# Performance work log

Measured on AMD Instinct MI355X. Metric: run time of the kernel, lower is better.

## Reference

```python
import jax, jax.numpy as jnp
import numpy as np

DIM = 64
DIM_BAK = 64
WIN = 8
HEADS = 4
HEAD_DIM = DIM // HEADS
SCALE = HEAD_DIM ** -0.5


def setup_inputs() -> dict:
    key = jax.random.key(0)
    ks = jax.random.split(key, 10)
    b, h, w = 8, 256, 256
    inp = {
        "query_feature": jax.random.normal(ks[0], (b, DIM, h, w), jnp.float32),
        "key_value_feature": jax.random.normal(ks[1], (b, DIM_BAK, h, w), jnp.float32),
        # Linear weights stored as (in, out); torch nn.Linear is y = x @ W.T + b
        "wq": jax.random.normal(ks[2], (DIM, DIM), jnp.float32) * 0.02,
        "bq": jnp.zeros((DIM,), jnp.float32),
        "wkv": jax.random.normal(ks[3], (DIM_BAK, 2 * DIM), jnp.float32) * 0.02,
        "bkv": jnp.zeros((2 * DIM,), jnp.float32),
        # depthwise 3x3 conv, groups=DIM_BAK, no bias; OIHW with I=1
        "w_dw": jax.random.normal(ks[4], (DIM_BAK, 1, 3, 3), jnp.float32) * 0.1,
        "w_out": jax.random.normal(ks[5], (DIM, DIM), jnp.float32) * 0.02,
        "b_out": jnp.zeros((DIM,), jnp.float32),
    }
    return inp


def _window_partition(x_nhwc, ws):
    # [B,H,W,C] -> [B*(H/ws)*(W/ws), ws*ws, C]
    B, H, W, C = x_nhwc.shape
    x = x_nhwc.reshape(B, H // ws, ws, W // ws, ws, C)
    x = x.transpose(0, 1, 3, 2, 4, 5)
    return x.reshape(-1, ws * ws, C)


def _window_reverse(win, ws, B, H, W):
    # [B*(H/ws)*(W/ws), ws, ws, C] -> [B,H,W,C]
    C = win.shape[-1]
    x = win.reshape(B, H // ws, W // ws, ws, ws, C)
    x = x.transpose(0, 1, 3, 2, 4, 5)
    return x.reshape(B, H, W, C)


def reference(query_feature, key_value_feature, wq, bq, wkv, bkv, w_dw, w_out, b_out):
    b, c, h, w = query_feature.shape
    c2 = key_value_feature.shape[1]

    # depthwise 3x3 conv on kv feature (NCHW)
    kv_feat = jax.lax.conv_general_dilated(
        key_value_feature, w_dw, window_strides=(1, 1), padding="SAME",
        dimension_numbers=("NCHW", "OIHW", "NCHW"), feature_group_count=c2)

    q_win = _window_partition(query_feature.transpose(0, 2, 3, 1), WIN)   # [B_, N, c]
    kv_win = _window_partition(kv_feat.transpose(0, 2, 3, 1), WIN)        # [B_, N, c2]
    B_, N, _ = q_win.shape

    q = (q_win @ wq + bq).reshape(B_, N, HEADS, HEAD_DIM).transpose(0, 2, 1, 3) * SCALE
    kv = (kv_win @ wkv + bkv).reshape(B_, N, 2, HEADS, HEAD_DIM).transpose(2, 0, 3, 1, 4)
    k, v = kv[0], kv[1]                                                   # [B_, H, N, hd]

    attn = jax.nn.softmax(jnp.einsum("bhnd,bhmd->bhnm", q, k), axis=-1)
    out = jnp.einsum("bhnm,bhmd->bhnd", attn, v)
    out = out.transpose(0, 2, 1, 3).reshape(B_, N, HEADS * HEAD_DIM)
    out = out @ w_out + b_out

    out = _window_reverse(out.reshape(-1, WIN, WIN, c), WIN, b, h, w)
    return out.transpose(0, 3, 1, 2)  # NCHW
```

## Files before the change

### kernel.cpp

```cpp
#include <hip/hip_runtime.h>
#include <hip/hip_bf16.h>

typedef __bf16 bf16x8 __attribute__((ext_vector_type(8)));
typedef float  f32x4  __attribute__((ext_vector_type(4)));
typedef short  s16x4  __attribute__((ext_vector_type(4)));

#define QSCALE 0.25f
#define LOG2E  1.4426950408889634f

static __device__ __forceinline__ unsigned short f2bf(float x) {
  union { __bf16 h; unsigned short u; } c;
  c.h = (__bf16)x;
  return c.u;
}
static __device__ __forceinline__ unsigned pk2(float a, float b) {
  union { __bf16 h[2]; unsigned u; } c;
  c.h[0] = (__bf16)a; c.h[1] = (__bf16)b;
  return c.u;
}
static __device__ __forceinline__ s16x4 mk4(unsigned w0, unsigned w1) {
  union { unsigned u[2]; s16x4 v; } c; c.u[0] = w0; c.u[1] = w1; return c.v;
}

#define SWZ(tk, ch2b) ((unsigned)((tk) * 128 + ((ch2b) ^ (((tk) & 7) << 4))))
#define OFFQ 15360u
#define OFFC 23552u

__global__ void prep_weights(const float* __restrict__ wq, const float* __restrict__ wkv,
                             const float* __restrict__ wout, const float* __restrict__ bq,
                             const float* __restrict__ bkv, const float* __restrict__ bout,
                             const float* __restrict__ wdw, unsigned* __restrict__ ws32) {
  const unsigned t = threadIdx.x;
  for (unsigned e = t; e < 2048; e += 256) {
    const unsigned fid = e >> 6, lane = e & 63;
    const unsigned l15 = lane & 15, g = lane >> 4;
    float v[8];
    if (fid < 8) {
      const unsigned nt = fid >> 1, kt = fid & 1, n = nt * 16 + l15;
#pragma unroll
      for (int i = 0; i < 8; ++i) v[i] = wq[(kt * 32 + g * 8 + i) * 64 + n] * (QSCALE * LOG2E);
    } else if (fid < 24) {
      const unsigned f = fid - 8, nt = f >> 1, kt = f & 1, n = nt * 16 + l15;
#pragma unroll
      for (int i = 0; i < 8; ++i) v[i] = wkv[(kt * 32 + g * 8 + i) * 128 + n];
    } else {
      const unsigned f = fid - 24, mt = f >> 1, kt = f & 1, m = mt * 16 + l15;
#pragma unroll
      for (int i = 0; i < 8; ++i) v[i] = wout[(kt * 32 + g * 8 + i) * 64 + m];
    }
#pragma unroll
    for (int w = 0; w < 4; ++w) ws32[e * 4 + w] = pk2(v[2 * w], v[2 * w + 1]);
  }
  float* bws = (float*)(ws32 + 8192);
  if (t < 64)       bws[t] = bq[t] * (QSCALE * LOG2E);
  else if (t < 192) bws[t] = bkv[t - 64];
  else if (t < 256) bws[t] = bout[t - 192];
  float* wT = (float*)(ws32 + 8448);
  for (unsigned e = t; e < 576; e += 256) {
    const unsigned k = e >> 6, ch = e & 63;
    wT[k * 64 + ch] = wdw[ch * 9 + k];
  }
}

__launch_bounds__(256, 5)
__global__ void fused_win_attn(const float* __restrict__ qf, const float* __restrict__ kvf,
                               const unsigned* __restrict__ ws32, float* __restrict__ out) {
  __shared__ __align__(16) char lds[31744];
  unsigned short* lds16 = (unsigned short*)lds;
  unsigned* lds32p = (unsigned*)lds;

  const unsigned bid = blockIdx.x;
  const unsigned wid = (bid & 7) * 1024 + (bid >> 3);
  const unsigned b = wid >> 10, rem = wid & 1023;
  const unsigned y0 = (rem >> 5) * 8, x0 = (rem & 31) * 8;

  const unsigned t = threadIdx.x;
  const unsigned lane = t & 63;
  const unsigned wv = t >> 6;
  const unsigned l15 = lane & 15, g = lane >> 4;
  const f32x4 zero4 = (f32x4){0.f, 0.f, 0.f, 0.f};

#pragma unroll
  for (int k = 0; k < 4; ++k) {
    const unsigned slot = (unsigned)k * 256 + t, seg = slot >> 1, part = slot & 1;
    const unsigned ch = seg >> 3, row = seg & 7;
    const f32x4 v = *(const f32x4*)(qf + ((size_t)b * 64 + ch) * 65536
                                    + (size_t)(y0 + row) * 256 + x0 + part * 4);
#pragma unroll
    for (int i = 0; i < 4; ++i)
      lds16[(OFFQ + SWZ(row * 8 + part * 4 + (unsigned)i, ch * 2)) >> 1] = f2bf(v[i]);
  }

#pragma unroll
  for (int k = 0; k < 10; ++k) {
    const unsigned slot = (unsigned)k * 256 + t, seg = slot >> 2, p4 = slot & 3;
    const unsigned irow = seg >> 6, ch = seg & 63;
    const int yy = (int)(y0 + irow) - 1;
    const int xs = (int)x0 - 4 + (int)p4 * 4;
    f32x4 v = zero4;
    if (yy >= 0 && yy < 256 && xs >= 0 && xs + 3 < 256)
      v = *(const f32x4*)(kvf + ((size_t)b * 64 + ch) * 65536 + (size_t)yy * 256 + xs);
    const unsigned base = irow * 384;
    if (p4 == 0) {
      lds32p[base + 0 * 64 + (ch & 63)]        = pk2(v[2], v[3]);
    } else if (p4 == 1) {
      lds32p[base + 1 * 64 + ((ch + 4) & 63)]  = pk2(v[0], v[1]);
      lds32p[base + 2 * 64 + ((ch + 8) & 63)]  = pk2(v[2], v[3]);
    } else if (p4 == 2) {
      lds32p[base + 3 * 64 + ((ch + 12) & 63)] = pk2(v[0], v[1]);
      lds32p[base + 4 * 64 + ((ch + 16) & 63)] = pk2(v[2], v[3]);
    } else {
      lds32p[base + 5 * 64 + ((ch + 20) & 63)] = pk2(v[0], v[1]);
    }
  }
  __syncthreads();

  {
    const unsigned ch = lane;
    const float* wT = (const float*)(ws32 + 8448);
    float wgt[9];
#pragma unroll
    for (int k2 = 0; k2 < 9; ++k2) wgt[k2] = wT[k2 * 64 + ch];
    float acc[2][8];
#pragma unroll
    for (int o = 0; o < 2; ++o)
#pragma unroll
      for (int c = 0; c < 8; ++c) acc[o][c] = 0.f;
#pragma unroll
    for (int il = 0; il < 4; ++il) {
      const unsigned irow = 2 * wv + (unsigned)il;
      float x[12];
#pragma unroll
      for (int j = 0; j < 6; ++j) {
        const unsigned u = lds32p[irow * 384 + (unsigned)j * 64 + ((ch + 4 * (unsigned)j) & 63)];
        x[2 * j]     = __uint_as_float(u << 16);
        x[2 * j + 1] = __uint_as_float(u & 0xffff0000u);
      }
#pragma unroll
      for (int o = 0; o < 2; ++o) {
        const int dr = il - o;
        if (dr >= 0 && dr <= 2) {
#pragma unroll
          for (int c = 0; c < 8; ++c)
            acc[o][c] = fmaf(x[c + 1], wgt[dr * 3],
                        fmaf(x[c + 2], wgt[dr * 3 + 1],
                        fmaf(x[c + 3], wgt[dr * 3 + 2], acc[o][c])));
        }
      }
    }
#pragma unroll
    for (int o = 0; o < 2; ++o)
#pragma unroll
      for (int c = 0; c < 8; ++c)
        lds16[(OFFC + SWZ((2 * wv + (unsigned)o) * 8 + (unsigned)c, ch * 2)) >> 1] =
            f2bf(acc[o][c]);
  }
  __syncthreads();

  const bf16x8* wsf = (const bf16x8*)ws32;
  const float* bws = (const float*)(ws32 + 8192);

  f32x4 qT[4], kT[4], vN[4];
  {
    const f32x4 bq4 = (f32x4){bws[wv * 16 + g * 4 + 0], bws[wv * 16 + g * 4 + 1],
                              bws[wv * 16 + g * 4 + 2], bws[wv * 16 + g * 4 + 3]};
    const f32x4 bk4 = (f32x4){bws[64 + wv * 16 + g * 4 + 0], bws[64 + wv * 16 + g * 4 + 1],
                              bws[64 + wv * 16 + g * 4 + 2], bws[64 + wv * 16 + g * 4 + 3]};
    const float bvv = bws[128 + wv * 16 + l15];
#pragma unroll
    for (int nt = 0; nt < 4; ++nt) {
      qT[nt] = bq4; kT[nt] = bk4;
      vN[nt] = (f32x4){bvv, bvv, bvv, bvv};
    }
#pragma unroll
    for (int kt = 0; kt < 2; ++kt) {
      const bf16x8 wqA = wsf[(wv * 2 + kt) * 64 + lane];
      const bf16x8 wkA = wsf[512 + (wv * 2 + kt) * 64 + lane];
      const bf16x8 wvB = wsf[512 + ((4 + wv) * 2 + kt) * 64 + lane];
#pragma unroll
      for (int nt = 0; nt < 4; ++nt) {
        const unsigned byo = SWZ(nt * 16 + l15, (kt * 32 + g * 8) * 2);
        const bf16x8 qF  = *(const bf16x8*)(lds + OFFQ + byo);
        const bf16x8 kvF = *(const bf16x8*)(lds + OFFC + byo);
        qT[nt] = __builtin_amdgcn_mfma_f32_16x16x32_bf16(wqA, qF,  qT[nt], 0, 0, 0);
        kT[nt] = __builtin_amdgcn_mfma_f32_16x16x32_bf16(wkA, kvF, kT[nt], 0, 0, 0);
        vN[nt] = __builtin_amdgcn_mfma_f32_16x16x32_bf16(kvF, wvB, vN[nt], 0, 0, 0);
      }
    }
  }

  unsigned ka[4][2], qa[4][2], va[4][2];
#pragma unroll
  for (int t4 = 0; t4 < 4; ++t4) {
    ka[t4][0] = pk2(kT[t4][0], kT[t4][1]); ka[t4][1] = pk2(kT[t4][2], kT[t4][3]);
    qa[t4][0] = pk2(qT[t4][0], qT[t4][1]); qa[t4][1] = pk2(qT[t4][2], qT[t4][3]);
    va[t4][0] = pk2(vN[t4][0], vN[t4][1]); va[t4][1] = pk2(vN[t4][2], vN[t4][3]);
  }

#pragma unroll
  for (int nt = 0; nt < 4; ++nt) {
    f32x4 s[4];
#pragma unroll
    for (int mt = 0; mt < 4; ++mt)
      s[mt] = __builtin_amdgcn_mfma_f32_16x16x16bf16_1k(
          mk4(ka[mt][0], ka[mt][1]), mk4(qa[nt][0], qa[nt][1]), zero4, 0, 0, 0);
    float m = s[0][0];
#pragma unroll
    for (int mt = 0; mt < 4; ++mt)
#pragma unroll
      for (int r = 0; r < 4; ++r) m = fmaxf(m, s[mt][r]);
    m = fmaxf(m, __shfl_xor(m, 16));
    m = fmaxf(m, __shfl_xor(m, 32));
    float sum = 0.f;
#pragma unroll
    for (int mt = 0; mt < 4; ++mt)
#pragma unroll
      for (int r = 0; r < 4; ++r) {
        const float e = exp2f(s[mt][r] - m);
        s[mt][r] = e;
        sum += e;
      }
    sum += __shfl_xor(sum, 16);
    sum += __shfl_xor(sum, 32);
    const float sinv = 1.0f / sum;
    f32x4 o = zero4;
#pragma unroll
    for (int k2 = 0; k2 < 4; ++k2)
      o = __builtin_amdgcn_mfma_f32_16x16x16bf16_1k(
          mk4(va[k2][0], va[k2][1]),
          mk4(pk2(s[k2][0], s[k2][1]), pk2(s[k2][2], s[k2][3])), o, 0, 0, 0);
#pragma unroll
    for (int r = 0; r < 4; ++r)
      lds16[SWZ(nt * 16 + l15, (wv * 16 + g * 4 + r) * 2) >> 1] = f2bf(o[r] * sinv);
  }
  __syncthreads();

  float bo[4];
#pragma unroll
  for (int r = 0; r < 4; ++r) bo[r] = bws[192 + wv * 16 + g * 4 + r];
  f32x4 facc[4];
#pragma unroll
  for (int nt = 0; nt < 4; ++nt) facc[nt] = (f32x4){bo[0], bo[1], bo[2], bo[3]};
#pragma unroll
  for (int kt = 0; kt < 2; ++kt) {
    const bf16x8 woA = wsf[1536 + (wv * 2 + kt) * 64 + lane];
#pragma unroll
    for (int nt = 0; nt < 4; ++nt) {
      const bf16x8 aB = *(const bf16x8*)(lds + SWZ(nt * 16 + l15, (kt * 32 + g * 8) * 2));
      facc[nt] = __builtin_amdgcn_mfma_f32_16x16x32_bf16(woA, aB, facc[nt], 0, 0, 0);
    }
  }
  float* ob = out + (size_t)b * 4194304 + (size_t)(wv * 16) * 65536 + (size_t)y0 * 256 + x0;
#pragma unroll
  for (int nt = 0; nt < 4; ++nt)
#pragma unroll
    for (int r = 0; r < 4; ++r) {
      const unsigned tk = nt * 16 + l15;
      ob[(size_t)(g * 4 + r) * 65536 + (tk >> 3) * 256 + (tk & 7)] = facc[nt][r];
    }
}

extern "C" void kernel_launch(void* const* d_in, const int* in_sizes, int n_in,
                              void* d_out, int out_size, void* d_ws, size_t ws_size,
                              hipStream_t stream) {
  const float* qf   = (const float*)d_in[0];
  const float* kvf  = (const float*)d_in[1];
  const float* wq   = (const float*)d_in[2];
  const float* bq   = (const float*)d_in[3];
  const float* wkv  = (const float*)d_in[4];
  const float* bkv  = (const float*)d_in[5];
  const float* wdw  = (const float*)d_in[6];
  const float* wout = (const float*)d_in[7];
  const float* bout = (const float*)d_in[8];
  (void)in_sizes; (void)n_in; (void)out_size; (void)ws_size;

  prep_weights<<<1, 256, 0, stream>>>(wq, wkv, wout, bq, bkv, bout, wdw, (unsigned*)d_ws);
  fused_win_attn<<<8192, 256, 0, stream>>>(qf, kvf, (const unsigned*)d_ws, (float*)d_out);
}
```

Before: 172.2 us.

## Switch depthwise conv and KV path to packed fp16 with edge-window fallback

The depthwise 3x3 conv now works on packed half2 values with hfma2 and alignbit shifts, and the K/V projections use fp16 MFMA on fp16 weights. Windows on the image border take a separate path that computes the conv straight from global memory with masking. The Q projection is moved ahead of the barrier so it overlaps the conv, and prep_weights is split across 9 blocks. This cuts conv ALU work and pack/unpack overhead, but fp16 has less range than bf16 and the edge path adds scattered global loads.

```diff
diff --git a/kernel.cpp b/kernel.cpp
--- a/kernel.cpp
+++ b/kernel.cpp
@@ -1,9 +1,11 @@
 #include <hip/hip_runtime.h>
 #include <hip/hip_bf16.h>
-
-typedef __bf16 bf16x8 __attribute__((ext_vector_type(8)));
-typedef float  f32x4  __attribute__((ext_vector_type(4)));
-typedef short  s16x4  __attribute__((ext_vector_type(4)));
+#include <hip/hip_fp16.h>
+
+typedef __bf16    bf16x8 __attribute__((ext_vector_type(8)));
+typedef _Float16  f16x8  __attribute__((ext_vector_type(8)));
+typedef float     f32x4  __attribute__((ext_vector_type(4)));
+typedef short     s16x4  __attribute__((ext_vector_type(4)));
 
 #define QSCALE 0.25f
 #define LOG2E  1.4426950408889634f
@@ -18,8 +20,19 @@
   c.h[0] = (__bf16)a; c.h[1] = (__bf16)b;
   return c.u;
 }
+static __device__ __forceinline__ unsigned pkh2(float a, float b) {
+  union { _Float16 h[2]; unsigned u; } c;
+  c.h[0] = (_Float16)a; c.h[1] = (_Float16)b;
+  return c.u;
+}
 static __device__ __forceinline__ s16x4 mk4(unsigned w0, unsigned w1) {
   union { unsigned u[2]; s16x4 v; } c; c.u[0] = w0; c.u[1] = w1; return c.v;
+}
+static __device__ __forceinline__ __half2 u2h2(unsigned u) {
+  union { unsigned u; __half2 h; } c; c.u = u; return c.h;
+}
+static __device__ __forceinline__ unsigned h2u(__half2 h) {
+  union { __half2 h; unsigned u; } c; c.h = h; return c.u;
 }
 
 #define SWZ(tk, ch2b) ((unsigned)((tk) * 128 + ((ch2b) ^ (((tk) & 7) << 4))))
@@ -30,11 +43,13 @@
                              const float* __restrict__ wout, const float* __restrict__ bq,
                              const float* __restrict__ bkv, const float* __restrict__ bout,
                              const float* __restrict__ wdw, unsigned* __restrict__ ws32) {
-  const unsigned t = threadIdx.x;
-  for (unsigned e = t; e < 2048; e += 256) {
+  const unsigned t = threadIdx.x, bid = blockIdx.x;
+  if (bid < 8) {
+    const unsigned e = bid * 256 + t;
     const unsigned fid = e >> 6, lane = e & 63;
     const unsigned l15 = lane & 15, g = lane >> 4;
     float v[8];
+    bool asF16 = false;
     if (fid < 8) {
       const unsigned nt = fid >> 1, kt = fid & 1, n = nt * 16 + l15;
 #pragma unroll
@@ -43,22 +58,31 @@
       const unsigned f = fid - 8, nt = f >> 1, kt = f & 1, n = nt * 16 + l15;
 #pragma unroll
       for (int i = 0; i < 8; ++i) v[i] = wkv[(kt * 32 + g * 8 + i) * 128 + n];
+      asF16 = true;
     } else {
       const unsigned f = fid - 24, mt = f >> 1, kt = f & 1, m = mt * 16 + l15;
 #pragma unroll
       for (int i = 0; i < 8; ++i) v[i] = wout[(kt * 32 + g * 8 + i) * 64 + m];
     }
-#pragma unroll
-    for (int w = 0; w < 4; ++w) ws32[e * 4 + w] = pk2(v[2 * w], v[2 * w + 1]);
-  }
-  float* bws = (float*)(ws32 + 8192);
-  if (t < 64)       bws[t] = bq[t] * (QSCALE * LOG2E);
-  else if (t < 192) bws[t] = bkv[t - 64];
-  else if (t < 256) bws[t] = bout[t - 192];
-  float* wT = (float*)(ws32 + 8448);
-  for (unsigned e = t; e < 576; e += 256) {
-    const unsigned k = e >> 6, ch = e & 63;
-    wT[k * 64 + ch] = wdw[ch * 9 + k];
+    if (asF16) {
+#pragma unroll
+      for (int w = 0; w < 4; ++w) ws32[e * 4 + w] = pkh2(v[2 * w], v[2 * w + 1]);
+    } else {
+#pragma unroll
+      for (int w = 0; w < 4; ++w) ws32[e * 4 + w] = pk2(v[2 * w], v[2 * w + 1]);
+    }
+  } else {
+    float* bws = (float*)(ws32 + 8192);
+    if (t < 64)       bws[t] = bq[t] * (QSCALE * LOG2E);
+    else if (t < 192) bws[t] = bkv[t - 64];
+    else if (t < 256) bws[t] = bout[t - 192];
+    float* wT = (float*)(ws32 + 8448);
+    for (unsigned e = t; e < 576; e += 256) {
+      const unsigned k = e >> 6, ch = e & 63;
+      const float w = wdw[ch * 9 + k];
+      wT[k * 64 + ch] = w;
+      ws32[9024 + k * 64 + ch] = pkh2(w, w);
+    }
   }
 }
 
@@ -102,99 +126,150 @@
       v = *(const f32x4*)(kvf + ((size_t)b * 64 + ch) * 65536 + (size_t)yy * 256 + xs);
     const unsigned base = irow * 384;
     if (p4 == 0) {
-      lds32p[base + 0 * 64 + (ch & 63)]        = pk2(v[2], v[3]);
+      lds32p[base + 0 * 64 + (ch & 63)]        = pkh2(v[2], v[3]);
     } else if (p4 == 1) {
-      lds32p[base + 1 * 64 + ((ch + 4) & 63)]  = pk2(v[0], v[1]);
-      lds32p[base + 2 * 64 + ((ch + 8) & 63)]  = pk2(v[2], v[3]);
+      lds32p[base + 1 * 64 + ((ch + 4) & 63)]  = pkh2(v[0], v[1]);
+      lds32p[base + 2 * 64 + ((ch + 8) & 63)]  = pkh2(v[2], v[3]);
     } else if (p4 == 2) {
-      lds32p[base + 3 * 64 + ((ch + 12) & 63)] = pk2(v[0], v[1]);
-      lds32p[base + 4 * 64 + ((ch + 16) & 63)] = pk2(v[2], v[3]);
+      lds32p[base + 3 * 64 + ((ch + 12) & 63)] = pkh2(v[0], v[1]);
+      lds32p[base + 4 * 64 + ((ch + 16) & 63)] = pkh2(v[2], v[3]);
     } else {
-      lds32p[base + 5 * 64 + ((ch + 20) & 63)] = pk2(v[0], v[1]);
+      lds32p[base + 5 * 64 + ((ch + 20) & 63)] = pkh2(v[0], v[1]);
     }
   }
   __syncthreads();
 
-  {
+  const bf16x8* wsf = (const bf16x8*)ws32;
+  const f16x8*  wsh = (const f16x8*)ws32;
+  const float* bws = (const float*)(ws32 + 8192);
+  const bool edge = (y0 == 0) || (y0 == 248) || (x0 == 0) || (x0 == 248);
+
+  if (!edge) {
     const unsigned ch = lane;
-    const float* wT = (const float*)(ws32 + 8448);
-    float wgt[9];
-#pragma unroll
-    for (int k2 = 0; k2 < 9; ++k2) wgt[k2] = wT[k2 * 64 + ch];
-    float acc[2][8];
+    __half2 wgt[9];
+#pragma unroll
+    for (int k2 = 0; k2 < 9; ++k2) wgt[k2] = u2h2(ws32[9024 + k2 * 64 + ch]);
+    __half2 acc[2][4];
 #pragma unroll
     for (int o = 0; o < 2; ++o)
 #pragma unroll
-      for (int c = 0; c < 8; ++c) acc[o][c] = 0.f;
+      for (int p = 0; p < 4; ++p) acc[o][p] = u2h2(0u);
 #pragma unroll
     for (int il = 0; il < 4; ++il) {
       const unsigned irow = 2 * wv + (unsigned)il;
-      float x[12];
-#pragma unroll
-      for (int j = 0; j < 6; ++j) {
-        const unsigned u = lds32p[irow * 384 + (unsigned)j * 64 + ((ch + 4 * (unsigned)j) & 63)];
-        x[2 * j]     = __uint_as_float(u << 16);
-        x[2 * j + 1] = __uint_as_float(u & 0xffff0000u);
-      }
+      unsigned xp[6];
+#pragma unroll
+      for (int j = 0; j < 6; ++j)
+        xp[j] = lds32p[irow * 384 + (unsigned)j * 64 + ((ch + 4 * (unsigned)j) & 63)];
+      unsigned u0[5];
+#pragma unroll
+      for (int p = 0; p < 5; ++p) u0[p] = __builtin_amdgcn_alignbit(xp[p + 1], xp[p], 16);
 #pragma unroll
       for (int o = 0; o < 2; ++o) {
         const int dr = il - o;
         if (dr >= 0 && dr <= 2) {
 #pragma unroll
-          for (int c = 0; c < 8; ++c)
-            acc[o][c] = fmaf(x[c + 1], wgt[dr * 3],
-                        fmaf(x[c + 2], wgt[dr * 3 + 1],
-                        fmaf(x[c + 3], wgt[dr * 3 + 2], acc[o][c])));
+          for (int p = 0; p < 4; ++p) {
+            acc[o][p] = __hfma2(u2h2(u0[p]),     wgt[dr * 3 + 0], acc[o][p]);
+            acc[o][p] = __hfma2(u2h2(xp[p + 1]), wgt[dr * 3 + 1], acc[o][p]);
+            acc[o][p] = __hfma2(u2h2(u0[p + 1]), wgt[dr * 3 + 2], acc[o][p]);
+          }
         }
       }
     }
 #pragma unroll
     for (int o = 0; o < 2; ++o)
 #pragma unroll
-      for (int c = 0; c < 8; ++c)
-        lds16[(OFFC + SWZ((2 * wv + (unsigned)o) * 8 + (unsigned)c, ch * 2)) >> 1] =
-            f2bf(acc[o][c]);
-  }
-  __syncthreads();
-
-  const bf16x8* wsf = (const bf16x8*)ws32;
-  const float* bws = (const float*)(ws32 + 8192);
-
-  f32x4 qT[4], kT[4], vN[4];
+      for (int p = 0; p < 4; ++p) {
+        const unsigned a = h2u(acc[o][p]);
+        const unsigned tok = (2 * wv + (unsigned)o) * 8 + 2 * (unsigned)p;
+        lds16[(OFFC + SWZ(tok, ch * 2)) >> 1]     = (unsigned short)(a & 0xffffu);
+        lds16[(OFFC + SWZ(tok + 1, ch * 2)) >> 1] = (unsigned short)(a >> 16);
+      }
+  } else {
+    const unsigned tok = lane;
+    const int yy = (int)(y0 + (tok >> 3)), xx = (int)(x0 + (tok & 7));
+    int off[9]; float msk[9];
+#pragma unroll
+    for (int dy = -1; dy <= 1; ++dy)
+#pragma unroll
+      for (int dx = -1; dx <= 1; ++dx) {
+        const int k = (dy + 1) * 3 + (dx + 1);
+        int yq = yy + dy, xq = xx + dx;
+        const bool ok = (yq >= 0) && (yq < 256) && (xq >= 0) && (xq < 256);
+        yq = yq < 0 ? 0 : (yq > 255 ? 255 : yq);
+        xq = xq < 0 ? 0 : (xq > 255 ? 255 : xq);
+        off[k] = yq * 256 + xq;
+        msk[k] = ok ? 1.f : 0.f;
+      }
+    const float* kb = kvf + (size_t)b * 4194304 + (size_t)(wv * 16) * 65536;
+    const float* wT = (const float*)(ws32 + 8448);
+#pragma unroll
+    for (int c2 = 0; c2 < 8; ++c2) {
+      float acc[2];
+#pragma unroll
+      for (int hh = 0; hh < 2; ++hh) {
+        const unsigned ch = wv * 16 + (unsigned)c2 * 2 + (unsigned)hh;
+        const float* cb = kb + (size_t)(c2 * 2 + hh) * 65536;
+        float a = 0.f;
+#pragma unroll
+        for (int k = 0; k < 9; ++k) a = fmaf(cb[off[k]], wT[k * 64 + ch] * msk[k], a);
+        acc[hh] = a;
+      }
+      lds32p[(OFFC + SWZ(tok, (wv * 16 + c2 * 2) * 2)) >> 2] = pkh2(acc[0], acc[1]);
+    }
+  }
+
+  unsigned qa[4][2];
   {
     const f32x4 bq4 = (f32x4){bws[wv * 16 + g * 4 + 0], bws[wv * 16 + g * 4 + 1],
                               bws[wv * 16 + g * 4 + 2], bws[wv * 16 + g * 4 + 3]};
+    f32x4 qT[4];
+#pragma unroll
+    for (int nt = 0; nt < 4; ++nt) qT[nt] = bq4;
+#pragma unroll
+    for (int kt = 0; kt < 2; ++kt) {
+      const bf16x8 wqA = wsf[(wv * 2 + kt) * 64 + lane];
+#pragma unroll
+      for (int nt = 0; nt < 4; ++nt) {
+        const bf16x8 qF = *(const bf16x8*)(lds + OFFQ + SWZ(nt * 16 + l15, (kt * 32 + g * 8) * 2));
+        qT[nt] = __builtin_amdgcn_mfma_f32_16x16x32_bf16(wqA, qF, qT[nt], 0, 0, 0);
+      }
+    }
+#pragma unroll
+    for (int t4 = 0; t4 < 4; ++t4) {
+      qa[t4][0] = pk2(qT[t4][0], qT[t4][1]); qa[t4][1] = pk2(qT[t4][2], qT[t4][3]);
+    }
+  }
+  __syncthreads();
+
+  unsigned ka[4][2], va[4][2];
+  {
     const f32x4 bk4 = (f32x4){bws[64 + wv * 16 + g * 4 + 0], bws[64 + wv * 16 + g * 4 + 1],
                               bws[64 + wv * 16 + g * 4 + 2], bws[64 + wv * 16 + g * 4 + 3]};
     const float bvv = bws[128 + wv * 16 + l15];
+    f32x4 kT[4], vN[4];
 #pragma unroll
     for (int nt = 0; nt < 4; ++nt) {
-      qT[nt] = bq4; kT[nt] = bk4;
+      kT[nt] = bk4;
       vN[nt] = (f32x4){bvv, bvv, bvv, bvv};
     }
 #pragma unroll
     for (int kt = 0; kt < 2; ++kt) {
-      const bf16x8 wqA = wsf[(wv * 2 + kt) * 64 + lane];
-      const bf16x8 wkA = wsf[512 + (wv * 2 + kt) * 64 + lane];
-      const bf16x8 wvB = wsf[512 + ((4 + wv) * 2 + kt) * 64 + lane];
+      const f16x8 wkA = wsh[512 + (wv * 2 + kt) * 64 + lane];
+      const f16x8 wvB = wsh[512 + ((4 + wv) * 2 + kt) * 64 + lane];
 #pragma unroll
       for (int nt = 0; nt < 4; ++nt) {
-        const unsigned byo = SWZ(nt * 16 + l15, (kt * 32 + g * 8) * 2);
-        const bf16x8 qF  = *(const bf16x8*)(lds + OFFQ + byo);
-        const bf16x8 kvF = *(const bf16x8*)(lds + OFFC + byo);
-        qT[nt] = __builtin_amdgcn_mfma_f32_16x16x32_bf16(wqA, qF,  qT[nt], 0, 0, 0);
-        kT[nt] = __builtin_amdgcn_mfma_f32_16x16x32_bf16(wkA, kvF, kT[nt], 0, 0, 0);
-        vN[nt] = __builtin_amdgcn_mfma_f32_16x16x32_bf16(kvF, wvB, vN[nt], 0, 0, 0);
-      }
-    }
-  }
-
-  unsigned ka[4][2], qa[4][2], va[4][2];
-#pragma unroll
-  for (int t4 = 0; t4 < 4; ++t4) {
-    ka[t4][0] = pk2(kT[t4][0], kT[t4][1]); ka[t4][1] = pk2(kT[t4][2], kT[t4][3]);
-    qa[t4][0] = pk2(qT[t4][0], qT[t4][1]); qa[t4][1] = pk2(qT[t4][2], qT[t4][3]);
-    va[t4][0] = pk2(vN[t4][0], vN[t4][1]); va[t4][1] = pk2(vN[t4][2], vN[t4][3]);
+        const f16x8 kvF = *(const f16x8*)(lds + OFFC + SWZ(nt * 16 + l15, (kt * 32 + g * 8) * 2));
+        kT[nt] = __builtin_amdgcn_mfma_f32_16x16x32_f16(wkA, kvF, kT[nt], 0, 0, 0);
+        vN[nt] = __builtin_amdgcn_mfma_f32_16x16x32_f16(kvF, wvB, vN[nt], 0, 0, 0);
+      }
+    }
+#pragma unroll
+    for (int t4 = 0; t4 < 4; ++t4) {
+      ka[t4][0] = pk2(kT[t4][0], kT[t4][1]); ka[t4][1] = pk2(kT[t4][2], kT[t4][3]);
+      va[t4][0] = pk2(vN[t4][0], vN[t4][1]); va[t4][1] = pk2(vN[t4][2], vN[t4][3]);
+    }
   }
 
 #pragma unroll
@@ -274,6 +349,6 @@
   const float* bout = (const float*)d_in[8];
   (void)in_sizes; (void)n_in; (void)out_size; (void)ws_size;
 
-  prep_weights<<<1, 256, 0, stream>>>(wq, wkv, wout, bq, bkv, bout, wdw, (unsigned*)d_ws);
+  prep_weights<<<9, 256, 0, stream>>>(wq, wkv, wout, bq, bkv, bout, wdw, (unsigned*)d_ws);
   fused_win_attn<<<8192, 256, 0, stream>>>(qf, kvf, (const unsigned*)d_ws, (float*)d_out);
 }
```

Measured after the change: 189.9 us. 10.3% more time.
